# Kernel optimization log

Hardware: AMD Instinct MI355X
Metric: run time of the kernel (lower is better)

## Reference

```python
import jax, jax.numpy as jnp
import numpy as np

N_NODES = 40000
N_EDGES = 640000
D = 128
BN_EPS = 1e-5
GATE_EPS = 1e-6


def _linear_params(key, d_in, d_out):
    kw, kb = jax.random.split(key)
    bound = 1.0 / np.sqrt(d_in)
    W = jax.random.uniform(kw, (d_out, d_in), jnp.float32, -bound, bound)
    b = jax.random.uniform(kb, (d_out,), jnp.float32, -bound, bound)
    return W, b


def setup_inputs() -> dict:
    key = jax.random.key(0)
    ks = jax.random.split(key, 8)
    x = jax.random.normal(ks[0], (N_NODES, D), jnp.float32)
    edge_index = jax.random.randint(ks[1], (2, N_EDGES), 0, N_NODES, jnp.int64)
    edge_attr = jax.random.normal(ks[2], (N_EDGES, D), jnp.float32)
    W_src_gate, b_src_gate = _linear_params(ks[3], D, D)
    W_dst_gate, b_dst_gate = _linear_params(ks[4], D, D)
    W_edge_gate, b_edge_gate = _linear_params(ks[5], D, D)
    W_src_update, b_src_update = _linear_params(ks[6], D, D)
    W_dst_update, b_dst_update = _linear_params(ks[7], D, D)
    return dict(
        x=x, edge_index=edge_index, edge_attr=edge_attr,
        W_src_gate=W_src_gate, b_src_gate=b_src_gate,
        W_dst_gate=W_dst_gate, b_dst_gate=b_dst_gate,
        W_edge_gate=W_edge_gate, b_edge_gate=b_edge_gate,
        W_src_update=W_src_update, b_src_update=b_src_update,
        W_dst_update=W_dst_update, b_dst_update=b_dst_update,
        bn_nodes_gamma=jnp.ones((D,), jnp.float32), bn_nodes_beta=jnp.zeros((D,), jnp.float32),
        bn_edges_gamma=jnp.ones((D,), jnp.float32), bn_edges_beta=jnp.zeros((D,), jnp.float32),
    )


def _batch_norm(z, gamma, beta):
    # training-mode BN: batch mean, biased variance (torch semantics)
    mean = jnp.mean(z, axis=0)
    var = jnp.mean(jnp.square(z - mean), axis=0)
    return gamma * (z - mean) * jax.lax.rsqrt(var + BN_EPS) + beta


def reference(x, edge_index, edge_attr,
              W_src_gate, b_src_gate, W_dst_gate, b_dst_gate,
              W_edge_gate, b_edge_gate, W_src_update, b_src_update,
              W_dst_update, b_dst_update,
              bn_nodes_gamma, bn_nodes_beta, bn_edges_gamma, bn_edges_beta):
    row, col = edge_index[0], edge_index[1]
    num_nodes = x.shape[0]
    x_row = x[row]                      # [E, D] gather
    x_col = x[col]                      # [E, D] gather
    e_src = x_row @ W_src_gate.T + b_src_gate
    e_dst = x_col @ W_dst_gate.T + b_dst_gate
    m = e_src + e_dst + edge_attr @ W_edge_gate.T + b_edge_gate  # [E, D]
    sigma = jax.nn.sigmoid(m)
    h_weighted = (x_col @ W_dst_update.T + b_dst_update) * sigma
    h_sum = jax.ops.segment_sum(h_weighted, col, num_segments=num_nodes)
    sigma_sum = jax.ops.segment_sum(sigma, col, num_segments=num_nodes)
    h_normalized = h_sum / (sigma_sum + GATE_EPS)
    x_new = x @ W_src_update.T + b_src_update + h_normalized
    x_new = jax.nn.softplus(_batch_norm(x_new, bn_nodes_gamma, bn_nodes_beta))
    y_new = jax.nn.softplus(_batch_norm(m, bn_edges_gamma, bn_edges_beta))
    x_new = x + x_new          # residual
    y_new = edge_attr + y_new  # residual
    return (x_new, y_new)
```

## Files before the change

kernel.cpp:

```cpp
#include <hip/hip_runtime.h>

#define NN 40000
#define NE 640000

typedef unsigned short u16;
typedef unsigned int u32;
typedef __attribute__((ext_vector_type(4))) float f32x4;
typedef __attribute__((ext_vector_type(4))) float fv4;
typedef __attribute__((ext_vector_type(4))) u32 uv4;
typedef __attribute__((ext_vector_type(8))) __bf16 bf16x8;

#define LSTR 136
#define TPW 8

__device__ __forceinline__ float bf2f(u16 u) { return __uint_as_float(((u32)u) << 16); }
__device__ __forceinline__ u16 f2bf(float f) {
  u32 u = __float_as_uint(f);
  u32 r = 0x7fffu + ((u >> 16) & 1u);
  return (u16)((u + r) >> 16);
}
__device__ __forceinline__ float splus(float v) {
  return fmaxf(v, 0.0f) + __logf(1.0f + __expf(-fabsf(v)));
}

__global__ void sniff_k(const u32* __restrict__ gamma, const u32* __restrict__ eidx,
                        u32* __restrict__ flags) {
  if (threadIdx.x == 0) {
    flags[0] = (gamma[0] == 0x3F803F80u) ? 1u : 0u;
    u32 odd = eidx[1] | eidx[3] | eidx[5] | eidx[7] |
              eidx[9] | eidx[11] | eidx[13] | eidx[15];
    flags[1] = (odd == 0u) ? 1u : 0u;
  }
}

__device__ __forceinline__ int load_col(const void* eidx, int e, u32 i64) {
  int nc = i64 ? (int)((const u32*)eidx)[2 * ((size_t)NE + e)]
               : ((const int*)eidx)[NE + e];
  return min(max(nc, 0), NN - 1);
}
__device__ __forceinline__ int load_row(const void* eidx, int e, u32 i64) {
  int nr = i64 ? (int)((const u32*)eidx)[2 * (size_t)e]
               : ((const int*)eidx)[e];
  return min(max(nr, 0), NN - 1);
}

__global__ __launch_bounds__(256) void wconv5_k(
    const float* __restrict__ W0, const float* __restrict__ W1,
    const float* __restrict__ W2, const float* __restrict__ W3,
    const float* __restrict__ W4, u16* __restrict__ out) {
  int i = blockIdx.x * 256 + threadIdx.x;
  int mtx = blockIdx.y;
  const float* W = (mtx == 0) ? W0 : (mtx == 1) ? W1 : (mtx == 2) ? W2
                 : (mtx == 3) ? W3 : W4;
  out[mtx * 16384 + i] = f2bf(W[i]);
}

__global__ __launch_bounds__(256) void hist_k(const void* __restrict__ eidx,
                                              u32* __restrict__ cnt,
                                              const u32* __restrict__ flags) {
  int e = blockIdx.x * 256 + threadIdx.x;
  atomicAdd(&cnt[load_col(eidx, e, flags[1])], 1u);
}

__device__ __forceinline__ bf16x8 a_frag(const float* __restrict__ row, int kbase) {
  float4 f0 = *(const float4*)(row + kbase);
  float4 f1 = *(const float4*)(row + kbase + 4);
  bf16x8 a;
  a[0] = (__bf16)f0.x; a[1] = (__bf16)f0.y; a[2] = (__bf16)f0.z; a[3] = (__bf16)f0.w;
  a[4] = (__bf16)f1.x; a[5] = (__bf16)f1.y; a[6] = (__bf16)f1.z; a[7] = (__bf16)f1.w;
  return a;
}

__device__ __forceinline__ bf16x8 cvt8v(fv4 a, fv4 b) {
  bf16x8 r;
  r[0] = (__bf16)a[0]; r[1] = (__bf16)a[1]; r[2] = (__bf16)a[2]; r[3] = (__bf16)a[3];
  r[4] = (__bf16)b[0]; r[5] = (__bf16)b[1]; r[6] = (__bf16)b[2]; r[7] = (__bf16)b[3];
  return r;
}

__device__ __forceinline__ void gemm16(const bf16x8 af[4], const u16* __restrict__ Wb,
                                       const float* __restrict__ bias, int lane,
                                       f32x4 acc[8]) {
  int l15 = lane & 15, lk = lane >> 4;
#pragma unroll
  for (int n = 0; n < 8; ++n) {
    float bv = bias[n * 16 + l15];
    acc[n] = (f32x4){bv, bv, bv, bv};
  }
#pragma unroll
  for (int n = 0; n < 8; ++n) {
    const u16* bp = Wb + (size_t)(n * 16 + l15) * 128 + lk * 8;
#pragma unroll
    for (int k = 0; k < 4; ++k) {
      bf16x8 b = *(const bf16x8*)(bp + 32 * k);
      acc[n] = __builtin_amdgcn_mfma_f32_16x16x32_bf16(af[k], b, acc[n], 0, 0, 0);
    }
  }
}

__device__ __forceinline__ void store_tile(u16* __restrict__ out, int m0, int lane,
                                           const f32x4 acc[8]) {
  int l15 = lane & 15, lk = lane >> 4;
#pragma unroll
  for (int n = 0; n < 8; ++n)
#pragma unroll
    for (int r = 0; r < 4; ++r)
      out[(size_t)(m0 + lk * 4 + r) * 128 + n * 16 + l15] = f2bf(acc[n][r]);
}

__global__ __launch_bounds__(256) void node_gemm_k(
    const float* __restrict__ x, const u16* __restrict__ Wb,
    const float* __restrict__ B0, const float* __restrict__ B1,
    const float* __restrict__ B2, const float* __restrict__ B3,
    const u32* __restrict__ cnt,
    u16* __restrict__ o0, u16* __restrict__ o1,
    u16* __restrict__ o2, u16* __restrict__ o3,
    float* __restrict__ statsg) {
  __shared__ float red[256];
  int tid = threadIdx.x, lane = tid & 63, w = tid >> 6;
  for (int i = tid; i < 256; i += 256) red[i] = 0.f;
  __syncthreads();
  int m0 = blockIdx.x * 64 + w * 16;
  int l15 = lane & 15, lk = lane >> 4;
  const float* arow = x + (size_t)(m0 + l15) * 128;
  bf16x8 af[4];
#pragma unroll
  for (int k = 0; k < 4; ++k) af[k] = a_frag(arow, 32 * k + 8 * lk);
  f32x4 acc[8], accd[8];
  gemm16(af, Wb + 0 * 16384, B0, lane, acc);  store_tile(o0, m0, lane, acc);
  gemm16(af, Wb + 1 * 16384, B1, lane, acc);  store_tile(o1, m0, lane, acc);
  gemm16(af, Wb + 2 * 16384, B2, lane, accd); store_tile(o2, m0, lane, accd);
  gemm16(af, Wb + 3 * 16384, B3, lane, acc);  store_tile(o3, m0, lane, acc);
  float g[4];
#pragma unroll
  for (int r = 0; r < 4; ++r) g[r] = (cnt[m0 + lk * 4 + r] != 0u) ? 1.0f : 0.0f;
#pragma unroll
  for (int n = 0; n < 8; ++n) {
    float a1 = 0.f, a2 = 0.f;
#pragma unroll
    for (int r = 0; r < 4; ++r) {
      float zv = acc[n][r] + g[r] * accd[n][r];
      a1 += zv;
      a2 = fmaf(zv, zv, a2);
    }
    a1 += __shfl_xor(a1, 16); a1 += __shfl_xor(a1, 32);
    a2 += __shfl_xor(a2, 16); a2 += __shfl_xor(a2, 32);
    if (lk == 0) {
      atomicAdd(&red[n * 16 + l15], a1);
      atomicAdd(&red[128 + n * 16 + l15], a2);
    }
  }
  __syncthreads();
  for (int i = tid; i < 256; i += 256) atomicAdd(&statsg[256 + i], red[i]);
}

__global__ __launch_bounds__(256, 2) void edge_gemm_k(
    const float* __restrict__ ea, const u16* __restrict__ Wgb,
    const float* __restrict__ Bg,
    const u16* __restrict__ g_src, const u16* __restrict__ g_dst,
    const void* __restrict__ eidx,
    u16* __restrict__ mge, float* __restrict__ statsg,
    const u32* __restrict__ flags) {
  __shared__ __align__(16) u16 gbuf[4][16 * LSTR];
  __shared__ __align__(16) u16 Wl[16384];
  int tid = threadIdx.x, lane = tid & 63, w = tid >> 6;
  int l15 = lane & 15, lk = lane >> 4;
  int el = lane >> 2, c4 = lane & 3;
  u32 i64 = flags[1];

  {
    const u32* Wg32 = (const u32*)Wgb;
    u32* Wl32 = (u32*)Wl;
#pragma unroll
    for (int j = 0; j < 32; ++j) {
      int i2 = tid + 256 * j;
      int r = i2 >> 6, c2 = i2 & 63;
      int g = c2 >> 2, win = c2 & 3;
      Wl32[r * 64 + (((g ^ ((r & 7) << 1)) << 2) | win)] = Wg32[i2];
    }
  }
  __syncthreads();

  u16* gt = gbuf[w];
  int sw = (l15 & 7) << 1;

  float bias[8];
#pragma unroll
  for (int n = 0; n < 8; ++n) bias[n] = Bg[n * 16 + l15];

  float e1[8] = {0.f, 0.f, 0.f, 0.f, 0.f, 0.f, 0.f, 0.f};
  float e2[8] = {0.f, 0.f, 0.f, 0.f, 0.f, 0.f, 0.f, 0.f};

  int base = (blockIdx.x * 4 + w) * (TPW * 16);
  const float* aptr = ea + (size_t)(base + l15) * 128 + 8 * lk;

  fv4 tmp[8];
#pragma unroll
  for (int k = 0; k < 4; ++k) {
    tmp[2 * k]     = *(const fv4*)(aptr + 32 * k);
    tmp[2 * k + 1] = *(const fv4*)(aptr + 32 * k + 4);
  }
  bf16x8 af[4];
#pragma unroll
  for (int k = 0; k < 4; ++k) af[k] = cvt8v(tmp[2 * k], tmp[2 * k + 1]);

  for (int t = 0; t < TPW; ++t) {
    int e0 = base + t * 16;
    int eg = e0 + el;
    int grow = load_row(eidx, eg, i64);
    int gcol = load_col(eidx, eg, i64);
#pragma unroll
    for (int it = 0; it < 4; ++it) {
      uv4 gsv = *(const uv4*)(g_src + (size_t)grow * 128 + c4 * 8 + it * 32);
      uv4 gdv = *(const uv4*)(g_dst + (size_t)gcol * 128 + c4 * 8 + it * 32);
      const u16* sp = (const u16*)&gsv;
      const u16* dp = (const u16*)&gdv;
      u32 pk[4];
#pragma unroll
      for (int j = 0; j < 4; ++j) {
        u16 a = f2bf(bf2f(sp[2 * j]) + bf2f(dp[2 * j]));
        u16 b = f2bf(bf2f(sp[2 * j + 1]) + bf2f(dp[2 * j + 1]));
        pk[j] = (u32)a | ((u32)b << 16);
      }
      int ch = c4 + 4 * it;
      *(uint4*)(gt + el * LSTR + ch * 8) = make_uint4(pk[0], pk[1], pk[2], pk[3]);
    }
    if (t + 1 < TPW) {
      const float* anx = aptr + (size_t)(t + 1) * 16 * 128;
#pragma unroll
      for (int k = 0; k < 4; ++k) {
        tmp[2 * k]     = *(const fv4*)(anx + 32 * k);
        tmp[2 * k + 1] = *(const fv4*)(anx + 32 * k + 4);
      }
    }
    f32x4 acc[8];
#pragma unroll
    for (int n = 0; n < 8; ++n)
      acc[n] = (f32x4){bias[n], bias[n], bias[n], bias[n]};
#pragma unroll
    for (int n = 0; n < 8; ++n)
#pragma unroll
      for (int k = 0; k < 4; ++k) {
        bf16x8 b = *(const bf16x8*)(Wl + ((n * 16 + l15) << 7) +
                                    (((lk + 4 * k) ^ sw) << 3));
        acc[n] = __builtin_amdgcn_mfma_f32_16x16x32_bf16(af[k], b, acc[n], 0, 0, 0);
      }
#pragma unroll
    for (int n = 0; n < 8; ++n)
#pragma unroll
      for (int r = 0; r < 4; ++r) {
        int ix = (lk * 4 + r) * LSTR + n * 16 + l15;
        float mv = acc[n][r] + bf2f(gt[ix]);
        e1[n] += mv;
        e2[n] = fmaf(mv, mv, e2[n]);
        gt[ix] = f2bf(mv);
      }
    if (t + 1 < TPW) {
#pragma unroll
      for (int k = 0; k < 4; ++k) af[k] = cvt8v(tmp[2 * k], tmp[2 * k + 1]);
    }
#pragma unroll
    for (int it = 0; it < 4; ++it) {
      int ch = c4 + 4 * it;
      uint4 v = *(const uint4*)(gt + el * LSTR + ch * 8);
      *(uint4*)(mge + (size_t)(e0 + el) * 128 + ch * 8) = v;
    }
  }
#pragma unroll
  for (int n = 0; n < 8; ++n) {
    float s1 = e1[n], s2 = e2[n];
    s1 += __shfl_xor(s1, 16); s1 += __shfl_xor(s1, 32);
    s2 += __shfl_xor(s2, 16); s2 += __shfl_xor(s2, 32);
    if (lk == 0) {
      atomicAdd(&statsg[n * 16 + l15], s1);
      atomicAdd(&statsg[128 + n * 16 + l15], s2);
    }
  }
}

__global__ void stats_fin_k(const float* __restrict__ es1, const float* __restrict__ es2,
                            const float* __restrict__ ns1, const float* __restrict__ ns2,
                            const float* __restrict__ eg_, const float* __restrict__ eb_,
                            const float* __restrict__ ng_, const float* __restrict__ nb_,
                            float* __restrict__ params) {
  int d = threadIdx.x;
  float em = es1[d] * (1.0f / NE);
  float ev = fmaxf(es2[d] * (1.0f / NE) - em * em, 0.0f);
  float esc = eg_[d] * rsqrtf(ev + 1e-5f);
  params[d] = esc;
  params[128 + d] = eb_[d] - em * esc;
  float nm = ns1[d] * (1.0f / NN);
  float nv = fmaxf(ns2[d] * (1.0f / NN) - nm * nm, 0.0f);
  float nsc = ng_[d] * rsqrtf(nv + 1e-5f);
  params[256 + d] = nsc;
  params[384 + d] = nb_[d] - nm * nsc;
}

__global__ __launch_bounds__(256) void node_fin2_k(
    const float* __restrict__ x, const u16* __restrict__ us,
    const u16* __restrict__ ud, const u32* __restrict__ cnt,
    const float* __restrict__ params, float* __restrict__ out) {
  size_t t = (size_t)blockIdx.x * 256 + threadIdx.x;
  size_t base = t * 8;
  int d0 = (int)(base & 127);
  int n = (int)(t >> 4);
  float g = (cnt[n] != 0u) ? 1.0f : 0.0f;
  float4 xa = *(const float4*)(x + base);
  float4 xb = *(const float4*)(x + base + 4);
  float xv[8] = {xa.x, xa.y, xa.z, xa.w, xb.x, xb.y, xb.z, xb.w};
  uint4 usv = *(const uint4*)(us + base);
  uint4 udv = *(const uint4*)(ud + base);
  const u16* up = (const u16*)&usv;
  const u16* dp = (const u16*)&udv;
  float o[8];
#pragma unroll
  for (int j = 0; j < 8; ++j) {
    float z = bf2f(up[j]) + g * bf2f(dp[j]);
    float bnv = z * params[256 + d0 + j] + params[384 + d0 + j];
    o[j] = xv[j] + splus(bnv);
  }
  *(float4*)(out + base) = make_float4(o[0], o[1], o[2], o[3]);
  *(float4*)(out + base + 4) = make_float4(o[4], o[5], o[6], o[7]);
}

__global__ __launch_bounds__(256) void edge_fin_k(
    const float* __restrict__ edge_attr, const u16* __restrict__ mge,
    const float* __restrict__ params, float* __restrict__ out) {
  size_t t = (size_t)blockIdx.x * 256 + threadIdx.x;
  size_t base = t * 8;
  int d0 = (int)(base & 127);
  float4 ea = *(const float4*)(edge_attr + base);
  float4 eb = *(const float4*)(edge_attr + base + 4);
  float ev[8] = {ea.x, ea.y, ea.z, ea.w, eb.x, eb.y, eb.z, eb.w};
  uint4 mv_ = *(const uint4*)(mge + base);
  const u16* mp = (const u16*)&mv_;
  float o[8];
#pragma unroll
  for (int j = 0; j < 8; ++j) {
    float m = bf2f(mp[j]);
    float bnv = m * params[d0 + j] + params[128 + d0 + j];
    o[j] = ev[j] + splus(bnv);
  }
  *(float4*)(out + base) = make_float4(o[0], o[1], o[2], o[3]);
  *(float4*)(out + base + 4) = make_float4(o[4], o[5], o[6], o[7]);
}

extern "C" void kernel_launch(void* const* d_in, const int* in_sizes, int n_in,
                              void* d_out, int out_size, void* d_ws, size_t ws_size,
                              hipStream_t stream) {
  const float* x        = (const float*)d_in[0];
  const void*  eidx     = d_in[1];
  const float* edge_att = (const float*)d_in[2];
  const float* Wsg = (const float*)d_in[3];  const float* bsg = (const float*)d_in[4];
  const float* Wdg = (const float*)d_in[5];  const float* bdg = (const float*)d_in[6];
  const float* Weg = (const float*)d_in[7];  const float* beg = (const float*)d_in[8];
  const float* Wsu = (const float*)d_in[9];  const float* bsu = (const float*)d_in[10];
  const float* Wdu = (const float*)d_in[11]; const float* bdu = (const float*)d_in[12];
  const float* bng = (const float*)d_in[13]; const float* bnb = (const float*)d_in[14];
  const float* beg_g = (const float*)d_in[15]; const float* beb = (const float*)d_in[16];

  char* ws = (char*)d_ws;
  u16*   g_src  = (u16*)(ws + 0);
  u16*   g_dst  = (u16*)(ws + 10240000);
  u16*   u_dst  = (u16*)(ws + 20480000);
  u16*   u_src  = (u16*)(ws + 30720000);
  float* stats  = (float*)(ws + 40960000);
  u32*   flags  = (u32*)(ws + 40964096);
  u16*   wbuf   = (u16*)(ws + 40968192);
  u32*   cnt    = (u32*)(ws + 41132032);
  u16*   mge    = (u16*)(ws + 41292032);

  hipMemsetAsync(stats, 0, 4096, stream);
  hipMemsetAsync(cnt, 0, 160000, stream);

  sniff_k<<<1, 64, 0, stream>>>((const u32*)bng, (const u32*)eidx, flags);
  wconv5_k<<<dim3(64, 5), 256, 0, stream>>>(Wsg, Wdg, Wdu, Wsu, Weg, wbuf);
  hist_k<<<NE / 256, 256, 0, stream>>>(eidx, cnt, flags);
  node_gemm_k<<<NN / 64, 256, 0, stream>>>(x, wbuf, bsg, bdg, bdu, bsu, cnt,
                                           g_src, g_dst, u_dst, u_src, stats);
  edge_gemm_k<<<NE / (64 * TPW), 256, 0, stream>>>(edge_att, wbuf + 4 * 16384, beg,
                                                   g_src, g_dst, eidx,
                                                   mge, stats, flags);
  stats_fin_k<<<1, 128, 0, stream>>>(stats, stats + 128, stats + 256, stats + 384,
                                     beg_g, beb, bng, bnb, stats + 512);
  node_fin2_k<<<(NN * 128) / 2048, 256, 0, stream>>>(x, u_src, u_dst, cnt,
                                                     stats + 512, (float*)d_out);
  edge_fin_k<<<(NE * 128) / 2048, 256, 0, stream>>>(edge_att, mge, stats + 512,
                                                    (float*)d_out + (size_t)NN * 128);
}
```

Before: 515.0 us.

## Split edge gather-add out of edge GEMM into separate stats and finalize passes

```diff
diff --git a/kernel.cpp b/kernel.cpp
--- a/kernel.cpp
+++ b/kernel.cpp
@@ -7,7 +7,6 @@
 typedef unsigned int u32;
 typedef __attribute__((ext_vector_type(4))) float f32x4;
 typedef __attribute__((ext_vector_type(4))) float fv4;
-typedef __attribute__((ext_vector_type(4))) u32 uv4;
 typedef __attribute__((ext_vector_type(8))) __bf16 bf16x8;
 
 #define LSTR 136
@@ -156,17 +155,12 @@
 
 __global__ __launch_bounds__(256, 2) void edge_gemm_k(
     const float* __restrict__ ea, const u16* __restrict__ Wgb,
-    const float* __restrict__ Bg,
-    const u16* __restrict__ g_src, const u16* __restrict__ g_dst,
-    const void* __restrict__ eidx,
-    u16* __restrict__ mge, float* __restrict__ statsg,
-    const u32* __restrict__ flags) {
-  __shared__ __align__(16) u16 gbuf[4][16 * LSTR];
+    const float* __restrict__ Bg, u16* __restrict__ mge) {
+  __shared__ __align__(16) u16 mt[4][16 * LSTR];
   __shared__ __align__(16) u16 Wl[16384];
   int tid = threadIdx.x, lane = tid & 63, w = tid >> 6;
   int l15 = lane & 15, lk = lane >> 4;
   int el = lane >> 2, c4 = lane & 3;
-  u32 i64 = flags[1];
 
   {
     const u32* Wg32 = (const u32*)Wgb;
@@ -181,15 +175,12 @@
   }
   __syncthreads();
 
-  u16* gt = gbuf[w];
+  u16* mtw = mt[w];
   int sw = (l15 & 7) << 1;
 
   float bias[8];
 #pragma unroll
   for (int n = 0; n < 8; ++n) bias[n] = Bg[n * 16 + l15];
-
-  float e1[8] = {0.f, 0.f, 0.f, 0.f, 0.f, 0.f, 0.f, 0.f};
-  float e2[8] = {0.f, 0.f, 0.f, 0.f, 0.f, 0.f, 0.f, 0.f};
 
   int base = (blockIdx.x * 4 + w) * (TPW * 16);
   const float* aptr = ea + (size_t)(base + l15) * 128 + 8 * lk;
@@ -206,25 +197,6 @@
 
   for (int t = 0; t < TPW; ++t) {
     int e0 = base + t * 16;
-    int eg = e0 + el;
-    int grow = load_row(eidx, eg, i64);
-    int gcol = load_col(eidx, eg, i64);
-#pragma unroll
-    for (int it = 0; it < 4; ++it) {
-      uv4 gsv = *(const uv4*)(g_src + (size_t)grow * 128 + c4 * 8 + it * 32);
-      uv4 gdv = *(const uv4*)(g_dst + (size_t)gcol * 128 + c4 * 8 + it * 32);
-      const u16* sp = (const u16*)&gsv;
-      const u16* dp = (const u16*)&gdv;
-      u32 pk[4];
-#pragma unroll
-      for (int j = 0; j < 4; ++j) {
-        u16 a = f2bf(bf2f(sp[2 * j]) + bf2f(dp[2 * j]));
-        u16 b = f2bf(bf2f(sp[2 * j + 1]) + bf2f(dp[2 * j + 1]));
-        pk[j] = (u32)a | ((u32)b << 16);
-      }
-      int ch = c4 + 4 * it;
-      *(uint4*)(gt + el * LSTR + ch * 8) = make_uint4(pk[0], pk[1], pk[2], pk[3]);
-    }
     if (t + 1 < TPW) {
       const float* anx = aptr + (size_t)(t + 1) * 16 * 128;
 #pragma unroll
@@ -248,13 +220,8 @@
 #pragma unroll
     for (int n = 0; n < 8; ++n)
 #pragma unroll
-      for (int r = 0; r < 4; ++r) {
-        int ix = (lk * 4 + r) * LSTR + n * 16 + l15;
-        float mv = acc[n][r] + bf2f(gt[ix]);
-        e1[n] += mv;
-        e2[n] = fmaf(mv, mv, e2[n]);
-        gt[ix] = f2bf(mv);
-      }
+      for (int r = 0; r < 4; ++r)
+        mtw[(lk * 4 + r) * LSTR + n * 16 + l15] = f2bf(acc[n][r]);
     if (t + 1 < TPW) {
 #pragma unroll
       for (int k = 0; k < 4; ++k) af[k] = cvt8v(tmp[2 * k], tmp[2 * k + 1]);
@@ -262,20 +229,57 @@
 #pragma unroll
     for (int it = 0; it < 4; ++it) {
       int ch = c4 + 4 * it;
-      uint4 v = *(const uint4*)(gt + el * LSTR + ch * 8);
+      uint4 v = *(const uint4*)(mtw + el * LSTR + ch * 8);
       *(uint4*)(mge + (size_t)(e0 + el) * 128 + ch * 8) = v;
     }
   }
-#pragma unroll
-  for (int n = 0; n < 8; ++n) {
-    float s1 = e1[n], s2 = e2[n];
-    s1 += __shfl_xor(s1, 16); s1 += __shfl_xor(s1, 32);
-    s2 += __shfl_xor(s2, 16); s2 += __shfl_xor(s2, 32);
-    if (lk == 0) {
-      atomicAdd(&statsg[n * 16 + l15], s1);
-      atomicAdd(&statsg[128 + n * 16 + l15], s2);
-    }
-  }
+}
+
+__global__ __launch_bounds__(256) void edge_stats_k(
+    const u16* __restrict__ mge, const void* __restrict__ eidx,
+    const u16* __restrict__ g_src, const u16* __restrict__ g_dst,
+    float* __restrict__ statsg, const u32* __restrict__ flags) {
+  __shared__ float red[256];
+  int tid = threadIdx.x, lane = tid & 63;
+  u32 i64 = flags[1];
+  int es = tid >> 4;
+  int d0 = (tid & 15) * 8;
+  for (int i = tid; i < 256; i += 256) red[i] = 0.f;
+  __syncthreads();
+  float s1[8] = {0.f, 0.f, 0.f, 0.f, 0.f, 0.f, 0.f, 0.f};
+  float s2[8] = {0.f, 0.f, 0.f, 0.f, 0.f, 0.f, 0.f, 0.f};
+  int base = blockIdx.x * 256;
+  for (int k = 0; k < 16; ++k) {
+    int e = base + k * 16 + es;
+    int row = load_row(eidx, e, i64);
+    int col = load_col(eidx, e, i64);
+    uint4 mv = *(const uint4*)(mge + (size_t)e * 128 + d0);
+    uint4 sv = *(const uint4*)(g_src + (size_t)row * 128 + d0);
+    uint4 dv = *(const uint4*)(g_dst + (size_t)col * 128 + d0);
+    const u16* mp = (const u16*)&mv;
+    const u16* sp = (const u16*)&sv;
+    const u16* dp = (const u16*)&dv;
+#pragma unroll
+    for (int j = 0; j < 8; ++j) {
+      float m = bf2f(mp[j]) + bf2f(sp[j]) + bf2f(dp[j]);
+      s1[j] += m;
+      s2[j] = fmaf(m, m, s2[j]);
+    }
+  }
+#pragma unroll
+  for (int j = 0; j < 8; ++j) {
+    s1[j] += __shfl_xor(s1[j], 16); s1[j] += __shfl_xor(s1[j], 32);
+    s2[j] += __shfl_xor(s2[j], 16); s2[j] += __shfl_xor(s2[j], 32);
+  }
+  if ((lane >> 4) == 0) {
+#pragma unroll
+    for (int j = 0; j < 8; ++j) {
+      atomicAdd(&red[d0 + j], s1[j]);
+      atomicAdd(&red[128 + d0 + j], s2[j]);
+    }
+  }
+  __syncthreads();
+  for (int i = tid; i < 256; i += 256) atomicAdd(&statsg[i], red[i]);
 }
 
 __global__ void stats_fin_k(const float* __restrict__ es1, const float* __restrict__ es2,
@@ -325,19 +329,30 @@
 
 __global__ __launch_bounds__(256) void edge_fin_k(
     const float* __restrict__ edge_attr, const u16* __restrict__ mge,
-    const float* __restrict__ params, float* __restrict__ out) {
+    const void* __restrict__ eidx,
+    const u16* __restrict__ g_src, const u16* __restrict__ g_dst,
+    const float* __restrict__ params, float* __restrict__ out,
+    const u32* __restrict__ flags) {
   size_t t = (size_t)blockIdx.x * 256 + threadIdx.x;
   size_t base = t * 8;
+  int e = (int)(t >> 4);
+  u32 i64 = flags[1];
+  int row = load_row(eidx, e, i64);
+  int col = load_col(eidx, e, i64);
   int d0 = (int)(base & 127);
   float4 ea = *(const float4*)(edge_attr + base);
   float4 eb = *(const float4*)(edge_attr + base + 4);
   float ev[8] = {ea.x, ea.y, ea.z, ea.w, eb.x, eb.y, eb.z, eb.w};
   uint4 mv_ = *(const uint4*)(mge + base);
+  uint4 gs_ = *(const uint4*)(g_src + (size_t)row * 128 + d0);
+  uint4 gd_ = *(const uint4*)(g_dst + (size_t)col * 128 + d0);
   const u16* mp = (const u16*)&mv_;
+  const u16* sp = (const u16*)&gs_;
+  const u16* dp = (const u16*)&gd_;
   float o[8];
 #pragma unroll
   for (int j = 0; j < 8; ++j) {
-    float m = bf2f(mp[j]);
+    float m = bf2f(mp[j]) + bf2f(sp[j]) + bf2f(dp[j]);
     float bnv = m * params[d0 + j] + params[128 + d0 + j];
     o[j] = ev[j] + splus(bnv);
   }
@@ -378,13 +393,14 @@
   hist_k<<<NE / 256, 256, 0, stream>>>(eidx, cnt, flags);
   node_gemm_k<<<NN / 64, 256, 0, stream>>>(x, wbuf, bsg, bdg, bdu, bsu, cnt,
                                            g_src, g_dst, u_dst, u_src, stats);
-  edge_gemm_k<<<NE / (64 * TPW), 256, 0, stream>>>(edge_att, wbuf + 4 * 16384, beg,
-                                                   g_src, g_dst, eidx,
-                                                   mge, stats, flags);
+  edge_gemm_k<<<NE / (64 * TPW), 256, 0, stream>>>(edge_att, wbuf + 4 * 16384, beg, mge);
+  edge_stats_k<<<NE / 256, 256, 0, stream>>>(mge, eidx, g_src, g_dst, stats, flags);
   stats_fin_k<<<1, 128, 0, stream>>>(stats, stats + 128, stats + 256, stats + 384,
                                      beg_g, beb, bng, bnb, stats + 512);
   node_fin2_k<<<(NN * 128) / 2048, 256, 0, stream>>>(x, u_src, u_dst, cnt,
                                                      stats + 512, (float*)d_out);
-  edge_fin_k<<<(NE * 128) / 2048, 256, 0, stream>>>(edge_att, mge, stats + 512,
-                                                    (float*)d_out + (size_t)NN * 128);
-}
+  edge_fin_k<<<(NE * 128) / 2048, 256, 0, stream>>>(edge_att, mge, eidx,
+                                                    g_src, g_dst, stats + 512,
+                                                    (float*)d_out + (size_t)NN * 128,
+                                                    flags);
+}
```

Measured after the change: 493.9 us. 1.04x faster.
